# Optimization experiments

Measured on AMD Instinct MI355X. Metric: run time of the kernel, lower is better.

The kernel has to match this reference:

```python
import jax, jax.numpy as jnp
import numpy as np
import math

B, A, IN_C, OUT_C = 64, 128, 128, 64

def _l2norm(x, eps=1e-12):
    # matches F.normalize(dim=1) on 2D input: x / max(||x||_2, eps) along last dim
    n = jnp.sqrt(jnp.sum(x * x, axis=-1, keepdims=True))
    return x / jnp.maximum(n, eps)

def setup_inputs() -> dict:
    key = jax.random.key(0)
    ks = jax.random.split(key, 7)
    s = 1.0 / math.sqrt(IN_C)
    return {
        "features": jax.random.normal(ks[0], (B, IN_C, A), dtype=jnp.float32),
        "Wq": jax.random.uniform(ks[1], (OUT_C, IN_C), jnp.float32, -s, s),
        "bq": jax.random.uniform(ks[2], (OUT_C,), jnp.float32, -s, s),
        "Wk": jax.random.uniform(ks[3], (OUT_C, IN_C), jnp.float32, -s, s),
        "bk": jax.random.uniform(ks[4], (OUT_C,), jnp.float32, -s, s),
        "Wv": jax.random.uniform(ks[5], (OUT_C, IN_C), jnp.float32, -s, s),
        "bv": jax.random.uniform(ks[6], (OUT_C,), jnp.float32, -s, s),
    }

def reference(features, Wq, bq, Wk, bk, Wv, bv):
    b = features.shape[0]
    f = jnp.transpose(features, (0, 2, 1))          # (b, a, in_c)
    a = f.shape[1]
    q = f @ Wq.T + bq                               # (b, a, d)
    k = f @ Wk.T + bk
    v = f @ Wv.T + bv
    d = q.shape[-1]
    qf = q.reshape(-1, d)                           # (N, d), N = b*a
    kf = k.reshape(-1, d)
    vf = v.reshape(-1, d)
    att = jax.nn.softmax(qf @ kf.T / math.sqrt(d), axis=1)  # (N, N)
    qkv = att @ vf                                  # (N, d)
    qkv_n = _l2norm(qkv).reshape(b, a, d)
    v_n = _l2norm(vf).reshape(b, a, d)
    # sim_s[i,j] = (1/a) * sum_t v_n[i,t] . qkv_n[j,t]  (diagonal-trace over 'a')
    sim_s = jnp.einsum('bad,cad->bc', v_n, qkv_n) / a
    return sim_s
```

## Files before the change

### kernel.cpp

```cpp
#include <hip/hip_runtime.h>
#include <hip/hip_bf16.h>

#define NROW 8192
#define INC  128
#define OUTC 64
#define BG   16

#define QSCALE 0.18033688011112042f

typedef __bf16 bf16x8 __attribute__((ext_vector_type(8)));
typedef __bf16 bf16x4 __attribute__((ext_vector_type(4)));
typedef short  s16x4  __attribute__((ext_vector_type(4)));
typedef short  s16x8  __attribute__((ext_vector_type(8)));
typedef float  f32x4  __attribute__((ext_vector_type(4)));

static __device__ __forceinline__ f32x4 mfma16(bf16x8 a, bf16x8 b, f32x4 c) {
    return __builtin_amdgcn_mfma_f32_16x16x32_bf16(a, b, c, 0, 0, 0);
}
static __device__ __forceinline__ f32x4 mfma1k(s16x4 a, s16x4 b, f32x4 c) {
    return __builtin_amdgcn_mfma_f32_16x16x16bf16_1k(a, b, c, 0, 0, 0);
}

static __device__ __forceinline__ bf16x8 cvt8(float4 lo, float4 hi) {
    bf16x8 r;
    r[0] = (__bf16)lo.x; r[1] = (__bf16)lo.y; r[2] = (__bf16)lo.z; r[3] = (__bf16)lo.w;
    r[4] = (__bf16)hi.x; r[5] = (__bf16)hi.y; r[6] = (__bf16)hi.z; r[7] = (__bf16)hi.w;
    return r;
}
static __device__ __forceinline__ s16x4 vlo(s16x8 x) {
    return __builtin_shufflevector(x, x, 0, 1, 2, 3);
}
static __device__ __forceinline__ s16x4 vhi(s16x8 x) {
    return __builtin_shufflevector(x, x, 4, 5, 6, 7);
}

__global__ __launch_bounds__(256) void proj_kernel(
    const float* __restrict__ feat,
    const float* __restrict__ Wq, const float* __restrict__ bq,
    const float* __restrict__ Wk, const float* __restrict__ bk,
    const float* __restrict__ Wv, const float* __restrict__ bv,
    __hip_bfloat16* __restrict__ qbf, __hip_bfloat16* __restrict__ kbf,
    __hip_bfloat16* __restrict__ vbf, __hip_bfloat16* __restrict__ vnb)
{
    __shared__ float slab[32 * 132];
    __shared__ float vbuf[32 * 66];
    __shared__ float invb[32];

    const int blk = blockIdx.x;
    const int b   = blk >> 2;
    const int a0  = (blk & 3) * 32;
    const int r0  = b * 128 + a0;
    const float* fb = feat + (size_t)b * INC * 128;

    for (int i = threadIdx.x; i < 32 * 128; i += 256) {
        int c = i >> 5, a = i & 31;
        slab[a * 132 + c] = fb[c * 128 + a0 + a];
    }
    __syncthreads();

    const int w    = threadIdx.x >> 6;
    const int lane = threadIdx.x & 63;
    const int l16  = lane & 15;
    const int quad = lane >> 4;

    f32x4 acc[3][2];
    #pragma unroll
    for (int t = 0; t < 3; ++t)
        #pragma unroll
        for (int u = 0; u < 2; ++u)
            acc[t][u] = (f32x4){0.f, 0.f, 0.f, 0.f};

    #pragma unroll
    for (int kc = 0; kc < 4; ++kc) {
        const int k0 = kc * 32 + quad * 8;
        bf16x8 afr[2];
        #pragma unroll
        for (int u = 0; u < 2; ++u) {
            const float* ar = slab + (u * 16 + l16) * 132 + k0;
            afr[u] = cvt8(*(const float4*)ar, *(const float4*)(ar + 4));
        }
        #pragma unroll
        for (int t = 0; t < 3; ++t) {
            const int tile = w * 3 + t;
            const int mat  = tile >> 2;
            const float* W = (mat == 0) ? Wq : (mat == 1) ? Wk : Wv;
            const float* wr = W + ((tile & 3) * 16 + l16) * INC + k0;
            bf16x8 bfr = cvt8(*(const float4*)wr, *(const float4*)(wr + 4));
            #pragma unroll
            for (int u = 0; u < 2; ++u)
                acc[t][u] = mfma16(afr[u], bfr, acc[t][u]);
        }
    }

    #pragma unroll
    for (int t = 0; t < 3; ++t) {
        const int tile = w * 3 + t;
        const int mat  = tile >> 2;
        const int nt   = tile & 3;
        const float* bias = (mat == 0) ? bq : (mat == 1) ? bk : bv;
        const float bl = bias[nt * 16 + l16];
        if (mat == 0) {
            #pragma unroll
            for (int u = 0; u < 2; ++u) {
                const int base = ((((r0 >> 4) + u) * 4 + nt) << 8) + l16;
                #pragma unroll
                for (int r = 0; r < 4; ++r)
                    qbf[base + (quad * 4 + r) * 16] =
                        __float2bfloat16((acc[t][u][r] + bl) * QSCALE);
            }
        } else if (mat == 1) {
            const int kq = (r0 >> 5) * 2048 + (nt >> 1) * 512 +
                           ((nt & 1) * 2 + (l16 >> 3)) * 128 + quad * 32 + (l16 & 7);
            #pragma unroll
            for (int u = 0; u < 2; ++u)
                #pragma unroll
                for (int r = 0; r < 4; ++r)
                    kbf[kq + u * 1024 + r * 8] = __float2bfloat16(acc[t][u][r] + bl);
        } else {
            #pragma unroll
            for (int u = 0; u < 2; ++u)
                #pragma unroll
                for (int r = 0; r < 4; ++r)
                    vbuf[(u * 16 + quad * 4 + r) * 66 + nt * 16 + l16] = acc[t][u][r] + bl;
        }
    }
    __syncthreads();

    const int rl = threadIdx.x >> 3;
    const int jj = threadIdx.x & 7;
    float ss = 0.f;
    #pragma unroll
    for (int i = 0; i < 8; ++i) {
        float x = vbuf[rl * 66 + jj * 8 + i];
        ss += x * x;
    }
    ss += __shfl_xor(ss, 1, 64);
    ss += __shfl_xor(ss, 2, 64);
    ss += __shfl_xor(ss, 4, 64);
    if (jj == 0) invb[rl] = rsqrtf(fmaxf(ss, 1e-24f));
    __syncthreads();
    float inv = invb[rl];
    bf16x8 vp;
    #pragma unroll
    for (int i = 0; i < 8; ++i)
        vp[i] = (__bf16)(vbuf[rl * 66 + jj * 8 + i] * inv);
    *(bf16x8*)(vnb + (size_t)(r0 + rl) * 64 + jj * 8) = vp;

    const int tl = threadIdx.x & 15;
    const int n  = (threadIdx.x >> 4) & 3;
    const int s_ = threadIdx.x >> 6;
    bf16x8 pack;
    #pragma unroll
    for (int j = 0; j < 8; ++j) {
        int key = s_ * 8 + j;
        pack[j] = (__bf16)(vbuf[key * 66 + n * 16 + tl] * invb[key]);
    }
    const int e1 = (r0 >> 5) * 2048 + (s_ >> 1) * 1024 + (n >> 1) * 512 +
                   (s_ & 1) * 256 + tl * 8 + (n & 1) * 4;
    bf16x4 plo = __builtin_shufflevector(pack, pack, 0, 1, 2, 3);
    bf16x4 phi = __builtin_shufflevector(pack, pack, 4, 5, 6, 7);
    *(bf16x4*)(vbf + e1)       = plo;
    *(bf16x4*)(vbf + e1 + 128) = phi;
}

#define STAGE_W(BUF, KR, VR) do {                                            \
        *(float4*)((BUF) + stb) = KR;                                        \
        *(float4*)((BUF) + 4096 + stb) = VR; } while (0)
#define STAGE_L(KR, VR) do {                                                 \
        KR = *(const float4*)gk; VR = *(const float4*)gv;                    \
        gk += 4096; gv += 4096; } while (0)

#define COMPUTE(BUF) do {                                                    \
    const char* kbp = (BUF);                                                 \
    const char* vbp = (BUF) + 4096;                                          \
    bf16x8 k00 = *(const bf16x8*)(kbp + lb);                                 \
    bf16x8 k01 = *(const bf16x8*)(kbp + lb + 1024);                          \
    bf16x8 k10 = *(const bf16x8*)(kbp + lb + 2048);                          \
    bf16x8 k11 = *(const bf16x8*)(kbp + lb + 3072);                          \
    s16x8 W0 = *(const s16x8*)(vbp + lb);                                    \
    s16x8 W1 = *(const s16x8*)(vbp + lb + 1024);                             \
    s16x8 W2 = *(const s16x8*)(vbp + lb + 2048);                             \
    s16x8 W3 = *(const s16x8*)(vbp + lb + 3072);                             \
    const f32x4 zero = (f32x4){0.f, 0.f, 0.f, 0.f};                          \
    _Pragma("unroll")                                                        \
    for (int u = 0; u < 4; ++u) {                                            \
        f32x4 s0 = mfma16(k00, qf32[u][0], zero);                            \
        s0       = mfma16(k01, qf32[u][1], s0);                              \
        f32x4 s1 = mfma16(k10, qf32[u][0], zero);                            \
        s1       = mfma16(k11, qf32[u][1], s1);                              \
        union { bf16x4 v; s16x4 s; } pf0, pf1;                               \
        _Pragma("unroll")                                                    \
        for (int r = 0; r < 4; ++r) {                                        \
            float p0 = __builtin_amdgcn_exp2f(s0[r]);                        \
            float p1 = __builtin_amdgcn_exp2f(s1[r]);                        \
            lp[u] += p0 + p1;                                                \
            pf0.v[r] = (__bf16)p0;                                           \
            pf1.v[r] = (__bf16)p1;                                           \
        }                                                                    \
        of[u][0] = mfma1k(pf0.s, vlo(W0), of[u][0]);                         \
        of[u][0] = mfma1k(pf1.s, vlo(W2), of[u][0]);                         \
        of[u][1] = mfma1k(pf0.s, vhi(W0), of[u][1]);                         \
        of[u][1] = mfma1k(pf1.s, vhi(W2), of[u][1]);                         \
        of[u][2] = mfma1k(pf0.s, vlo(W1), of[u][2]);                         \
        of[u][2] = mfma1k(pf1.s, vlo(W3), of[u][2]);                         \
        of[u][3] = mfma1k(pf0.s, vhi(W1), of[u][3]);                         \
        of[u][3] = mfma1k(pf1.s, vhi(W3), of[u][3]);                         \
    } } while (0)

__global__ __launch_bounds__(256, 2) void attn_kernel(
    const __hip_bfloat16* __restrict__ qbf,
    const __hip_bfloat16* __restrict__ kbf,
    const __hip_bfloat16* __restrict__ vbf,
    float* __restrict__ Opart, float* __restrict__ lpart)
{
    __shared__ float4 ldsq[2][512];
    char* bufA = (char*)&ldsq[0][0];
    char* bufB = (char*)&ldsq[1][0];

    const int qb    = blockIdx.x >> 4;
    const int bg    = blockIdx.x & 15;
    const int tid   = threadIdx.x;
    const int w     = tid >> 6;
    const int lane  = tid & 63;
    const int l16   = lane & 15;
    const int quad  = lane >> 4;
    const int r0    = qb * 256 + w * 64;
    const int fo32  = l16 * 16 + (quad & 1) * 8;
    const int qh    = quad >> 1;
    const int lb    = lane * 16;
    const int stb   = tid * 16;

    bf16x8 qf32[4][2];
    #pragma unroll
    for (int u = 0; u < 4; ++u)
        #pragma unroll
        for (int p = 0; p < 2; ++p)
            qf32[u][p] = *(const bf16x8*)(qbf +
                ((((r0 >> 4) + u) * 4 + p * 2 + qh) << 8) + fo32);

    f32x4 of[4][4];
    float lp[4] = {0.f, 0.f, 0.f, 0.f};
    #pragma unroll
    for (int u = 0; u < 4; ++u)
        #pragma unroll
        for (int n = 0; n < 4; ++n)
            of[u][n] = (f32x4){0.f, 0.f, 0.f, 0.f};

    const char* gk = (const char*)kbf + (size_t)(bg * 16) * 4096 + stb;
    const char* gv = (const char*)vbf + (size_t)(bg * 16) * 4096 + stb;

    float4 ka, va, kb_, vb_;
    STAGE_L(ka, va);
    STAGE_W(bufA, ka, va);
    STAGE_L(kb_, vb_);
    __syncthreads();

    #pragma unroll 1
    for (int body = 0; body < 7; ++body) {
        STAGE_W(bufB, kb_, vb_);
        STAGE_L(ka, va);
        COMPUTE(bufA);
        __syncthreads();
        STAGE_W(bufA, ka, va);
        STAGE_L(kb_, vb_);
        COMPUTE(bufB);
        __syncthreads();
    }
    STAGE_W(bufB, kb_, vb_);
    COMPUTE(bufA);
    __syncthreads();
    COMPUTE(bufB);

    #pragma unroll
    for (int u = 0; u < 4; ++u) {
        float v = lp[u];
        v += __shfl_xor(v, 16, 64);
        v += __shfl_xor(v, 32, 64);
        lp[u] = v;
    }

    const int task = (qb * 4 + w) * 16 + bg;
    float* Ob = Opart + (size_t)task * 4096;
    #pragma unroll
    for (int u = 0; u < 4; ++u)
        #pragma unroll
        for (int n = 0; n < 4; ++n)
            #pragma unroll
            for (int r = 0; r < 4; ++r)
                Ob[(u * 16 + quad * 4 + r) * 64 + n * 16 + l16] = of[u][n][r];
    if (quad == 0) {
        #pragma unroll
        for (int u = 0; u < 4; ++u)
            lpart[task * 64 + u * 16 + l16] = lp[u];
    }
}

__global__ __launch_bounds__(256) void combine_kernel(
    const float* __restrict__ Opart, const float* __restrict__ lpart,
    __hip_bfloat16* __restrict__ qnb, float* __restrict__ outz)
{
    if (blockIdx.x == 0) {
        #pragma unroll
        for (int z = 0; z < 4; ++z)
            ((float4*)outz)[threadIdx.x * 4 + z] = (float4){0.f, 0.f, 0.f, 0.f};
    }

    const int r    = blockIdx.x * 4 + (threadIdx.x >> 6);
    const int c    = threadIdx.x & 63;
    const int tile = r >> 6, row = r & 63;
    float acc = 0.f, lsum = 0.f;
    #pragma unroll
    for (int g = 0; g < 16; ++g) {
        int task = tile * 16 + g;
        acc  += Opart[(size_t)task * 4096 + row * 64 + c];
        lsum += lpart[task * 64 + row];
    }
    float q = acc / lsum;
    float ss = q * q;
    ss += __shfl_xor(ss, 1, 64);
    ss += __shfl_xor(ss, 2, 64);
    ss += __shfl_xor(ss, 4, 64);
    ss += __shfl_xor(ss, 8, 64);
    ss += __shfl_xor(ss, 16, 64);
    ss += __shfl_xor(ss, 32, 64);
    qnb[(size_t)r * 64 + c] = __float2bfloat16(q * rsqrtf(fmaxf(ss, 1e-24f)));
}

__global__ __launch_bounds__(256) void sim_kernel(
    const __hip_bfloat16* __restrict__ vnb,
    const __hip_bfloat16* __restrict__ qnb,
    float* __restrict__ out)
{
    const int w    = threadIdx.x >> 6;
    const int lane = threadIdx.x & 63;
    const int l16  = lane & 15;
    const int quad = lane >> 4;
    const int k0   = blockIdx.x * 128 + w * 32 + quad * 8;

    f32x4 acc[4][4];
    #pragma unroll
    for (int mi = 0; mi < 4; ++mi)
        #pragma unroll
        for (int ni = 0; ni < 4; ++ni)
            acc[mi][ni] = (f32x4){0.f, 0.f, 0.f, 0.f};

    bf16x8 af[4], bfv[4];
    #pragma unroll
    for (int mi = 0; mi < 4; ++mi)
        af[mi] = *(const bf16x8*)(vnb + (size_t)(mi * 16 + l16) * 8192 + k0);
    #pragma unroll
    for (int ni = 0; ni < 4; ++ni)
        bfv[ni] = *(const bf16x8*)(qnb + (size_t)(ni * 16 + l16) * 8192 + k0);
    #pragma unroll
    for (int mi = 0; mi < 4; ++mi)
        #pragma unroll
        for (int ni = 0; ni < 4; ++ni)
            acc[mi][ni] = mfma16(af[mi], bfv[ni], acc[mi][ni]);

    #pragma unroll
    for (int mi = 0; mi < 4; ++mi)
        #pragma unroll
        for (int ni = 0; ni < 4; ++ni)
            #pragma unroll
            for (int r = 0; r < 4; ++r)
                atomicAdd(&out[(mi * 16 + quad * 4 + r) * 64 + ni * 16 + l16],
                          acc[mi][ni][r] * (1.f / 128.f));
}

extern "C" void kernel_launch(void* const* d_in, const int* in_sizes, int n_in,
                              void* d_out, int out_size, void* d_ws, size_t ws_size,
                              hipStream_t stream)
{
    const float* feat = (const float*)d_in[0];
    const float* Wq   = (const float*)d_in[1];
    const float* bq   = (const float*)d_in[2];
    const float* Wk   = (const float*)d_in[3];
    const float* bk   = (const float*)d_in[4];
    const float* Wv   = (const float*)d_in[5];
    const float* bv   = (const float*)d_in[6];
    float* out = (float*)d_out;

    const size_t MB = 1u << 20;
    char* ws = (char*)d_ws;
    __hip_bfloat16* qbf = (__hip_bfloat16*)(ws);
    __hip_bfloat16* kbf = (__hip_bfloat16*)(ws + 1 * MB);
    __hip_bfloat16* vbf = (__hip_bfloat16*)(ws + 2 * MB);
    __hip_bfloat16* vnb = (__hip_bfloat16*)(ws + 3 * MB);
    float* Opart = (float*)(ws + 4 * MB);
    float* lpart = (float*)(ws + 36 * MB);
    __hip_bfloat16* qnb = (__hip_bfloat16*)(ws + 37 * MB);

    proj_kernel<<<256, 256, 0, stream>>>(feat, Wq, bq, Wk, bk, Wv, bv, qbf, kbf, vbf, vnb);
    attn_kernel<<<512, 256, 0, stream>>>(qbf, kbf, vbf, Opart, lpart);
    combine_kernel<<<2048, 256, 0, stream>>>(Opart, lpart, qnb, out);
    sim_kernel<<<64, 256, 0, stream>>>(vnb, qnb, out);
}
```

Before: 121.6 us.

## Fuse all four stages into one cooperative kernel with grid syncs

Merges projection, attention, combine and similarity into a single cooperative launch of 512 blocks, separated by grid-wide barriers, and keeps the four-kernel path as a fallback if the cooperative launch fails. The aim is to remove the launch gaps and tail effects between the four kernel launches. The combine and similarity stages now run with fewer blocks looping over their work. Grid-sync cost and lower parallelism in the later stages may offset the savings.

```diff
diff --git a/kernel.cpp b/kernel.cpp
--- a/kernel.cpp
+++ b/kernel.cpp
@@ -1,5 +1,8 @@
 #include <hip/hip_runtime.h>
 #include <hip/hip_bf16.h>
+#include <hip/hip_cooperative_groups.h>
+
+namespace cg = cooperative_groups;
 
 #define NROW 8192
 #define INC  128
@@ -34,134 +37,6 @@
     return __builtin_shufflevector(x, x, 4, 5, 6, 7);
 }
 
-__global__ __launch_bounds__(256) void proj_kernel(
-    const float* __restrict__ feat,
-    const float* __restrict__ Wq, const float* __restrict__ bq,
-    const float* __restrict__ Wk, const float* __restrict__ bk,
-    const float* __restrict__ Wv, const float* __restrict__ bv,
-    __hip_bfloat16* __restrict__ qbf, __hip_bfloat16* __restrict__ kbf,
-    __hip_bfloat16* __restrict__ vbf, __hip_bfloat16* __restrict__ vnb)
-{
-    __shared__ float slab[32 * 132];
-    __shared__ float vbuf[32 * 66];
-    __shared__ float invb[32];
-
-    const int blk = blockIdx.x;
-    const int b   = blk >> 2;
-    const int a0  = (blk & 3) * 32;
-    const int r0  = b * 128 + a0;
-    const float* fb = feat + (size_t)b * INC * 128;
-
-    for (int i = threadIdx.x; i < 32 * 128; i += 256) {
-        int c = i >> 5, a = i & 31;
-        slab[a * 132 + c] = fb[c * 128 + a0 + a];
-    }
-    __syncthreads();
-
-    const int w    = threadIdx.x >> 6;
-    const int lane = threadIdx.x & 63;
-    const int l16  = lane & 15;
-    const int quad = lane >> 4;
-
-    f32x4 acc[3][2];
-    #pragma unroll
-    for (int t = 0; t < 3; ++t)
-        #pragma unroll
-        for (int u = 0; u < 2; ++u)
-            acc[t][u] = (f32x4){0.f, 0.f, 0.f, 0.f};
-
-    #pragma unroll
-    for (int kc = 0; kc < 4; ++kc) {
-        const int k0 = kc * 32 + quad * 8;
-        bf16x8 afr[2];
-        #pragma unroll
-        for (int u = 0; u < 2; ++u) {
-            const float* ar = slab + (u * 16 + l16) * 132 + k0;
-            afr[u] = cvt8(*(const float4*)ar, *(const float4*)(ar + 4));
-        }
-        #pragma unroll
-        for (int t = 0; t < 3; ++t) {
-            const int tile = w * 3 + t;
-            const int mat  = tile >> 2;
-            const float* W = (mat == 0) ? Wq : (mat == 1) ? Wk : Wv;
-            const float* wr = W + ((tile & 3) * 16 + l16) * INC + k0;
-            bf16x8 bfr = cvt8(*(const float4*)wr, *(const float4*)(wr + 4));
-            #pragma unroll
-            for (int u = 0; u < 2; ++u)
-                acc[t][u] = mfma16(afr[u], bfr, acc[t][u]);
-        }
-    }
-
-    #pragma unroll
-    for (int t = 0; t < 3; ++t) {
-        const int tile = w * 3 + t;
-        const int mat  = tile >> 2;
-        const int nt   = tile & 3;
-        const float* bias = (mat == 0) ? bq : (mat == 1) ? bk : bv;
-        const float bl = bias[nt * 16 + l16];
-        if (mat == 0) {
-            #pragma unroll
-            for (int u = 0; u < 2; ++u) {
-                const int base = ((((r0 >> 4) + u) * 4 + nt) << 8) + l16;
-                #pragma unroll
-                for (int r = 0; r < 4; ++r)
-                    qbf[base + (quad * 4 + r) * 16] =
-                        __float2bfloat16((acc[t][u][r] + bl) * QSCALE);
-            }
-        } else if (mat == 1) {
-            const int kq = (r0 >> 5) * 2048 + (nt >> 1) * 512 +
-                           ((nt & 1) * 2 + (l16 >> 3)) * 128 + quad * 32 + (l16 & 7);
-            #pragma unroll
-            for (int u = 0; u < 2; ++u)
-                #pragma unroll
-                for (int r = 0; r < 4; ++r)
-                    kbf[kq + u * 1024 + r * 8] = __float2bfloat16(acc[t][u][r] + bl);
-        } else {
-            #pragma unroll
-            for (int u = 0; u < 2; ++u)
-                #pragma unroll
-                for (int r = 0; r < 4; ++r)
-                    vbuf[(u * 16 + quad * 4 + r) * 66 + nt * 16 + l16] = acc[t][u][r] + bl;
-        }
-    }
-    __syncthreads();
-
-    const int rl = threadIdx.x >> 3;
-    const int jj = threadIdx.x & 7;
-    float ss = 0.f;
-    #pragma unroll
-    for (int i = 0; i < 8; ++i) {
-        float x = vbuf[rl * 66 + jj * 8 + i];
-        ss += x * x;
-    }
-    ss += __shfl_xor(ss, 1, 64);
-    ss += __shfl_xor(ss, 2, 64);
-    ss += __shfl_xor(ss, 4, 64);
-    if (jj == 0) invb[rl] = rsqrtf(fmaxf(ss, 1e-24f));
-    __syncthreads();
-    float inv = invb[rl];
-    bf16x8 vp;
-    #pragma unroll
-    for (int i = 0; i < 8; ++i)
-        vp[i] = (__bf16)(vbuf[rl * 66 + jj * 8 + i] * inv);
-    *(bf16x8*)(vnb + (size_t)(r0 + rl) * 64 + jj * 8) = vp;
-
-    const int tl = threadIdx.x & 15;
-    const int n  = (threadIdx.x >> 4) & 3;
-    const int s_ = threadIdx.x >> 6;
-    bf16x8 pack;
-    #pragma unroll
-    for (int j = 0; j < 8; ++j) {
-        int key = s_ * 8 + j;
-        pack[j] = (__bf16)(vbuf[key * 66 + n * 16 + tl] * invb[key]);
-    }
-    const int e1 = (r0 >> 5) * 2048 + (s_ >> 1) * 1024 + (n >> 1) * 512 +
-                   (s_ & 1) * 256 + tl * 8 + (n & 1) * 4;
-    bf16x4 plo = __builtin_shufflevector(pack, pack, 0, 1, 2, 3);
-    bf16x4 phi = __builtin_shufflevector(pack, pack, 4, 5, 6, 7);
-    *(bf16x4*)(vbf + e1)       = plo;
-    *(bf16x4*)(vbf + e1 + 128) = phi;
-}
 
 #define STAGE_W(BUF, KR, VR) do {                                            \
         *(float4*)((BUF) + stb) = KR;                                        \
@@ -207,92 +82,313 @@
         of[u][3] = mfma1k(pf1.s, vhi(W3), of[u][3]);                         \
     } } while (0)
 
+#define PROJ_BODY(BID)                                                       \
+    do {                                                                     \
+        const int b   = (BID) >> 2;                                          \
+        const int a0  = ((BID) & 3) * 32;                                    \
+        const int r0  = b * 128 + a0;                                        \
+        const float* fb = feat + (size_t)b * INC * 128;                      \
+        for (int i = tid; i < 32 * 128; i += 256) {                          \
+            int c = i >> 5, a = i & 31;                                      \
+            slab[a * 132 + c] = fb[c * 128 + a0 + a];                        \
+        }                                                                    \
+        __syncthreads();                                                     \
+        f32x4 acc[3][2];                                                     \
+        _Pragma("unroll")                                                    \
+        for (int t = 0; t < 3; ++t)                                          \
+            _Pragma("unroll")                                                \
+            for (int u = 0; u < 2; ++u)                                      \
+                acc[t][u] = (f32x4){0.f, 0.f, 0.f, 0.f};                     \
+        _Pragma("unroll")                                                    \
+        for (int kc = 0; kc < 4; ++kc) {                                     \
+            const int k0 = kc * 32 + quad * 8;                               \
+            bf16x8 afr[2];                                                   \
+            _Pragma("unroll")                                                \
+            for (int u = 0; u < 2; ++u) {                                    \
+                const float* ar = slab + (u * 16 + l16) * 132 + k0;          \
+                afr[u] = cvt8(*(const float4*)ar, *(const float4*)(ar + 4)); \
+            }                                                                \
+            _Pragma("unroll")                                                \
+            for (int t = 0; t < 3; ++t) {                                    \
+                const int tile = w * 3 + t;                                  \
+                const int mat  = tile >> 2;                                  \
+                const float* W = (mat == 0) ? Wq : (mat == 1) ? Wk : Wv;     \
+                const float* wr = W + ((tile & 3) * 16 + l16) * INC + k0;    \
+                bf16x8 bfr = cvt8(*(const float4*)wr, *(const float4*)(wr + 4)); \
+                _Pragma("unroll")                                            \
+                for (int u = 0; u < 2; ++u)                                  \
+                    acc[t][u] = mfma16(afr[u], bfr, acc[t][u]);              \
+            }                                                                \
+        }                                                                    \
+        _Pragma("unroll")                                                    \
+        for (int t = 0; t < 3; ++t) {                                        \
+            const int tile = w * 3 + t;                                      \
+            const int mat  = tile >> 2;                                      \
+            const int nt   = tile & 3;                                       \
+            const float* bias = (mat == 0) ? bq : (mat == 1) ? bk : bv;      \
+            const float bl = bias[nt * 16 + l16];                            \
+            if (mat == 0) {                                                  \
+                _Pragma("unroll")                                            \
+                for (int u = 0; u < 2; ++u) {                                \
+                    const int base = ((((r0 >> 4) + u) * 4 + nt) << 8) + l16;\
+                    _Pragma("unroll")                                        \
+                    for (int r = 0; r < 4; ++r)                              \
+                        qbf[base + (quad * 4 + r) * 16] =                    \
+                            __float2bfloat16((acc[t][u][r] + bl) * QSCALE);  \
+                }                                                            \
+            } else if (mat == 1) {                                           \
+                const int kq = (r0 >> 5) * 2048 + (nt >> 1) * 512 +          \
+                    ((nt & 1) * 2 + (l16 >> 3)) * 128 + quad * 32 + (l16 & 7);\
+                _Pragma("unroll")                                            \
+                for (int u = 0; u < 2; ++u)                                  \
+                    _Pragma("unroll")                                        \
+                    for (int r = 0; r < 4; ++r)                              \
+                        kbf[kq + u * 1024 + r * 8] =                         \
+                            __float2bfloat16(acc[t][u][r] + bl);             \
+            } else {                                                         \
+                _Pragma("unroll")                                            \
+                for (int u = 0; u < 2; ++u)                                  \
+                    _Pragma("unroll")                                        \
+                    for (int r = 0; r < 4; ++r)                              \
+                        vbuf[(u * 16 + quad * 4 + r) * 66 + nt * 16 + l16] = \
+                            acc[t][u][r] + bl;                               \
+            }                                                                \
+        }                                                                    \
+        __syncthreads();                                                     \
+        const int rl = tid >> 3;                                             \
+        const int jj = tid & 7;                                              \
+        float ss = 0.f;                                                      \
+        _Pragma("unroll")                                                    \
+        for (int i = 0; i < 8; ++i) {                                        \
+            float x = vbuf[rl * 66 + jj * 8 + i];                            \
+            ss += x * x;                                                     \
+        }                                                                    \
+        ss += __shfl_xor(ss, 1, 64);                                         \
+        ss += __shfl_xor(ss, 2, 64);                                         \
+        ss += __shfl_xor(ss, 4, 64);                                         \
+        if (jj == 0) invb[rl] = rsqrtf(fmaxf(ss, 1e-24f));                   \
+        __syncthreads();                                                     \
+        float inv = invb[rl];                                                \
+        bf16x8 vpk;                                                          \
+        _Pragma("unroll")                                                    \
+        for (int i = 0; i < 8; ++i)                                          \
+            vpk[i] = (__bf16)(vbuf[rl * 66 + jj * 8 + i] * inv);             \
+        *(bf16x8*)(vnb + (size_t)(r0 + rl) * 64 + jj * 8) = vpk;             \
+        const int tl = tid & 15;                                             \
+        const int n  = (tid >> 4) & 3;                                       \
+        const int s_ = tid >> 6;                                             \
+        bf16x8 pack;                                                         \
+        _Pragma("unroll")                                                    \
+        for (int j = 0; j < 8; ++j) {                                        \
+            int key = s_ * 8 + j;                                            \
+            pack[j] = (__bf16)(vbuf[key * 66 + n * 16 + tl] * invb[key]);    \
+        }                                                                    \
+        const int e1 = (r0 >> 5) * 2048 + (s_ >> 1) * 1024 + (n >> 1) * 512 +\
+                       (s_ & 1) * 256 + tl * 8 + (n & 1) * 4;                \
+        bf16x4 plo = __builtin_shufflevector(pack, pack, 0, 1, 2, 3);        \
+        bf16x4 phi = __builtin_shufflevector(pack, pack, 4, 5, 6, 7);        \
+        *(bf16x4*)(vbf + e1)       = plo;                                    \
+        *(bf16x4*)(vbf + e1 + 128) = phi;                                    \
+    } while (0)
+
+#define ATTN_BODY(BID, BUFA, BUFB)                                           \
+    do {                                                                     \
+        const int qb   = (BID) >> 4;                                         \
+        const int bg   = (BID) & 15;                                         \
+        const int r0   = qb * 256 + w * 64;                                  \
+        const int fo32 = l16 * 16 + (quad & 1) * 8;                          \
+        const int qh   = quad >> 1;                                          \
+        const int lb   = lane * 16;                                          \
+        const int stb  = tid * 16;                                           \
+        bf16x8 qf32[4][2];                                                   \
+        _Pragma("unroll")                                                    \
+        for (int u = 0; u < 4; ++u)                                          \
+            _Pragma("unroll")                                                \
+            for (int p = 0; p < 2; ++p)                                      \
+                qf32[u][p] = *(const bf16x8*)(qbf +                          \
+                    ((((r0 >> 4) + u) * 4 + p * 2 + qh) << 8) + fo32);       \
+        f32x4 of[4][4];                                                      \
+        float lp[4] = {0.f, 0.f, 0.f, 0.f};                                  \
+        _Pragma("unroll")                                                    \
+        for (int u = 0; u < 4; ++u)                                          \
+            _Pragma("unroll")                                                \
+            for (int n = 0; n < 4; ++n)                                      \
+                of[u][n] = (f32x4){0.f, 0.f, 0.f, 0.f};                      \
+        const char* gk = (const char*)kbf + (size_t)(bg * 16) * 4096 + stb;  \
+        const char* gv = (const char*)vbf + (size_t)(bg * 16) * 4096 + stb;  \
+        float4 ka, va, kb_, vb_;                                             \
+        STAGE_L(ka, va);                                                     \
+        STAGE_W(BUFA, ka, va);                                               \
+        STAGE_L(kb_, vb_);                                                   \
+        __syncthreads();                                                     \
+        _Pragma("unroll 1")                                                  \
+        for (int body = 0; body < 7; ++body) {                               \
+            STAGE_W(BUFB, kb_, vb_);                                         \
+            STAGE_L(ka, va);                                                 \
+            COMPUTE(BUFA);                                                   \
+            __syncthreads();                                                 \
+            STAGE_W(BUFA, ka, va);                                           \
+            STAGE_L(kb_, vb_);                                               \
+            COMPUTE(BUFB);                                                   \
+            __syncthreads();                                                 \
+        }                                                                    \
+        STAGE_W(BUFB, kb_, vb_);                                             \
+        COMPUTE(BUFA);                                                       \
+        __syncthreads();                                                     \
+        COMPUTE(BUFB);                                                       \
+        _Pragma("unroll")                                                    \
+        for (int u = 0; u < 4; ++u) {                                        \
+            float v = lp[u];                                                 \
+            v += __shfl_xor(v, 16, 64);                                      \
+            v += __shfl_xor(v, 32, 64);                                      \
+            lp[u] = v;                                                       \
+        }                                                                    \
+        const int task = (qb * 4 + w) * 16 + bg;                             \
+        float* Ob = Opart + (size_t)task * 4096;                             \
+        _Pragma("unroll")                                                    \
+        for (int u = 0; u < 4; ++u)                                          \
+            _Pragma("unroll")                                                \
+            for (int n = 0; n < 4; ++n)                                      \
+                _Pragma("unroll")                                            \
+                for (int r = 0; r < 4; ++r)                                  \
+                    Ob[(u * 16 + quad * 4 + r) * 64 + n * 16 + l16] =        \
+                        of[u][n][r];                                         \
+        if (quad == 0) {                                                     \
+            _Pragma("unroll")                                                \
+            for (int u = 0; u < 4; ++u)                                      \
+                lpart[task * 64 + u * 16 + l16] = lp[u];                     \
+        }                                                                    \
+    } while (0)
+
+__global__ __launch_bounds__(256, 2) void mega_kernel(
+    const float* __restrict__ feat,
+    const float* __restrict__ Wq, const float* __restrict__ bq,
+    const float* __restrict__ Wk, const float* __restrict__ bk,
+    const float* __restrict__ Wv, const float* __restrict__ bv,
+    __hip_bfloat16* __restrict__ qbf, __hip_bfloat16* __restrict__ kbf,
+    __hip_bfloat16* __restrict__ vbf, __hip_bfloat16* __restrict__ vnb,
+    float* __restrict__ Opart, float* __restrict__ lpart,
+    __hip_bfloat16* __restrict__ qnb, float* __restrict__ out)
+{
+    cg::grid_group gg = cg::this_grid();
+
+    __shared__ __align__(16) char pool[25472];
+
+    const int bid = blockIdx.x;
+    const int tid = threadIdx.x;
+    const int w    = tid >> 6;
+    const int lane = tid & 63;
+    const int l16  = lane & 15;
+    const int quad = lane >> 4;
+
+    if (bid < 256) {
+        float* slab = (float*)pool;
+        float* vbuf = (float*)(pool + 16896);
+        float* invb = (float*)(pool + 25344);
+        PROJ_BODY(bid);
+    }
+    __threadfence();
+    gg.sync();
+
+    {
+        char* bufA = pool;
+        char* bufB = pool + 8192;
+        ATTN_BODY(bid, bufA, bufB);
+    }
+    __threadfence();
+    gg.sync();
+
+    {
+        if (bid == 0) {
+            #pragma unroll
+            for (int z = 0; z < 4; ++z)
+                ((float4*)out)[tid * 4 + z] = (float4){0.f, 0.f, 0.f, 0.f};
+        }
+        #pragma unroll 1
+        for (int it = 0; it < 4; ++it) {
+            const int r    = (it * 512 + bid) * 4 + (tid >> 6);
+            const int c    = tid & 63;
+            const int tile = r >> 6, row = r & 63;
+            float acc = 0.f, lsum = 0.f;
+            #pragma unroll
+            for (int g = 0; g < 16; ++g) {
+                int task = tile * 16 + g;
+                acc  += Opart[(size_t)task * 4096 + row * 64 + c];
+                lsum += lpart[task * 64 + row];
+            }
+            float q = acc / lsum;
+            float ss = q * q;
+            ss += __shfl_xor(ss, 1, 64);
+            ss += __shfl_xor(ss, 2, 64);
+            ss += __shfl_xor(ss, 4, 64);
+            ss += __shfl_xor(ss, 8, 64);
+            ss += __shfl_xor(ss, 16, 64);
+            ss += __shfl_xor(ss, 32, 64);
+            qnb[(size_t)r * 64 + c] = __float2bfloat16(q * rsqrtf(fmaxf(ss, 1e-24f)));
+        }
+    }
+    __threadfence();
+    gg.sync();
+
+    if (bid < 256) {
+        const int k0 = bid * 32 + quad * 8;
+        f32x4 acc[4];
+        #pragma unroll
+        for (int ni = 0; ni < 4; ++ni)
+            acc[ni] = (f32x4){0.f, 0.f, 0.f, 0.f};
+
+        bf16x8 af = *(const bf16x8*)(vnb + (size_t)(w * 16 + l16) * 8192 + k0);
+        bf16x8 bfv[4];
+        #pragma unroll
+        for (int ni = 0; ni < 4; ++ni)
+            bfv[ni] = *(const bf16x8*)(qnb + (size_t)(ni * 16 + l16) * 8192 + k0);
+        #pragma unroll
+        for (int ni = 0; ni < 4; ++ni)
+            acc[ni] = mfma16(af, bfv[ni], acc[ni]);
+
+        #pragma unroll
+        for (int ni = 0; ni < 4; ++ni)
+            #pragma unroll
+            for (int r = 0; r < 4; ++r)
+                atomicAdd(&out[(w * 16 + quad * 4 + r) * 64 + ni * 16 + l16],
+                          acc[ni][r] * (1.f / 128.f));
+    }
+}
+
+__global__ __launch_bounds__(256) void proj_kernel(
+    const float* __restrict__ feat,
+    const float* __restrict__ Wq, const float* __restrict__ bq,
+    const float* __restrict__ Wk, const float* __restrict__ bk,
+    const float* __restrict__ Wv, const float* __restrict__ bv,
+    __hip_bfloat16* __restrict__ qbf, __hip_bfloat16* __restrict__ kbf,
+    __hip_bfloat16* __restrict__ vbf, __hip_bfloat16* __restrict__ vnb)
+{
+    __shared__ float slab[32 * 132];
+    __shared__ float vbuf[32 * 66];
+    __shared__ float invb[32];
+    const int tid = threadIdx.x;
+    const int w    = tid >> 6;
+    const int lane = tid & 63;
+    const int l16  = lane & 15;
+    const int quad = lane >> 4;
+    PROJ_BODY(blockIdx.x);
+}
+
 __global__ __launch_bounds__(256, 2) void attn_kernel(
     const __hip_bfloat16* __restrict__ qbf,
     const __hip_bfloat16* __restrict__ kbf,
     const __hip_bfloat16* __restrict__ vbf,
     float* __restrict__ Opart, float* __restrict__ lpart)
 {
-    __shared__ float4 ldsq[2][512];
-    char* bufA = (char*)&ldsq[0][0];
-    char* bufB = (char*)&ldsq[1][0];
-
-    const int qb    = blockIdx.x >> 4;
-    const int bg    = blockIdx.x & 15;
-    const int tid   = threadIdx.x;
-    const int w     = tid >> 6;
-    const int lane  = tid & 63;
-    const int l16   = lane & 15;
-    const int quad  = lane >> 4;
-    const int r0    = qb * 256 + w * 64;
-    const int fo32  = l16 * 16 + (quad & 1) * 8;
-    const int qh    = quad >> 1;
-    const int lb    = lane * 16;
-    const int stb   = tid * 16;
-
-    bf16x8 qf32[4][2];
-    #pragma unroll
-    for (int u = 0; u < 4; ++u)
-        #pragma unroll
-        for (int p = 0; p < 2; ++p)
-            qf32[u][p] = *(const bf16x8*)(qbf +
-                ((((r0 >> 4) + u) * 4 + p * 2 + qh) << 8) + fo32);
-
-    f32x4 of[4][4];
-    float lp[4] = {0.f, 0.f, 0.f, 0.f};
-    #pragma unroll
-    for (int u = 0; u < 4; ++u)
-        #pragma unroll
-        for (int n = 0; n < 4; ++n)
-            of[u][n] = (f32x4){0.f, 0.f, 0.f, 0.f};
-
-    const char* gk = (const char*)kbf + (size_t)(bg * 16) * 4096 + stb;
-    const char* gv = (const char*)vbf + (size_t)(bg * 16) * 4096 + stb;
-
-    float4 ka, va, kb_, vb_;
-    STAGE_L(ka, va);
-    STAGE_W(bufA, ka, va);
-    STAGE_L(kb_, vb_);
-    __syncthreads();
-
-    #pragma unroll 1
-    for (int body = 0; body < 7; ++body) {
-        STAGE_W(bufB, kb_, vb_);
-        STAGE_L(ka, va);
-        COMPUTE(bufA);
-        __syncthreads();
-        STAGE_W(bufA, ka, va);
-        STAGE_L(kb_, vb_);
-        COMPUTE(bufB);
-        __syncthreads();
-    }
-    STAGE_W(bufB, kb_, vb_);
-    COMPUTE(bufA);
-    __syncthreads();
-    COMPUTE(bufB);
-
-    #pragma unroll
-    for (int u = 0; u < 4; ++u) {
-        float v = lp[u];
-        v += __shfl_xor(v, 16, 64);
-        v += __shfl_xor(v, 32, 64);
-        lp[u] = v;
-    }
-
-    const int task = (qb * 4 + w) * 16 + bg;
-    float* Ob = Opart + (size_t)task * 4096;
-    #pragma unroll
-    for (int u = 0; u < 4; ++u)
-        #pragma unroll
-        for (int n = 0; n < 4; ++n)
-            #pragma unroll
-            for (int r = 0; r < 4; ++r)
-                Ob[(u * 16 + quad * 4 + r) * 64 + n * 16 + l16] = of[u][n][r];
-    if (quad == 0) {
-        #pragma unroll
-        for (int u = 0; u < 4; ++u)
-            lpart[task * 64 + u * 16 + l16] = lp[u];
-    }
+    __shared__ __align__(16) char pool[16384];
+    const int tid = threadIdx.x;
+    const int w    = tid >> 6;
+    const int lane = tid & 63;
+    const int l16  = lane & 15;
+    const int quad = lane >> 4;
+    char* bufA = pool;
+    char* bufB = pool + 8192;
+    ATTN_BODY(blockIdx.x, bufA, bufB);
 }
 
 __global__ __launch_bounds__(256) void combine_kernel(
@@ -304,7 +400,6 @@
         for (int z = 0; z < 4; ++z)
             ((float4*)outz)[threadIdx.x * 4 + z] = (float4){0.f, 0.f, 0.f, 0.f};
     }
-
     const int r    = blockIdx.x * 4 + (threadIdx.x >> 6);
     const int c    = threadIdx.x & 63;
     const int tile = r >> 6, row = r & 63;
@@ -390,8 +485,18 @@
     float* lpart = (float*)(ws + 36 * MB);
     __hip_bfloat16* qnb = (__hip_bfloat16*)(ws + 37 * MB);
 
-    proj_kernel<<<256, 256, 0, stream>>>(feat, Wq, bq, Wk, bk, Wv, bv, qbf, kbf, vbf, vnb);
-    attn_kernel<<<512, 256, 0, stream>>>(qbf, kbf, vbf, Opart, lpart);
-    combine_kernel<<<2048, 256, 0, stream>>>(Opart, lpart, qnb, out);
-    sim_kernel<<<64, 256, 0, stream>>>(vnb, qnb, out);
-}
+    void* args[] = {
+        (void*)&feat, (void*)&Wq, (void*)&bq, (void*)&Wk, (void*)&bk,
+        (void*)&Wv, (void*)&bv, (void*)&qbf, (void*)&kbf, (void*)&vbf,
+        (void*)&vnb, (void*)&Opart, (void*)&lpart, (void*)&qnb, (void*)&out
+    };
+    hipError_t err = hipLaunchCooperativeKernel((const void*)mega_kernel,
+                                                dim3(512), dim3(256), args, 0, stream);
+    if (err != hipSuccess) {
+        proj_kernel<<<256, 256, 0, stream>>>(feat, Wq, bq, Wk, bk, Wv, bv,
+                                             qbf, kbf, vbf, vnb);
+        attn_kernel<<<512, 256, 0, stream>>>(qbf, kbf, vbf, Opart, lpart);
+        combine_kernel<<<2048, 256, 0, stream>>>(Opart, lpart, qnb, out);
+        sim_kernel<<<64, 256, 0, stream>>>(vnb, qnb, out);
+    }
+}
```

Result: slower. 443.2 us (+264.4%).

## Fuse split-K combine with similarity kernel and relayout partial outputs

Applied to the files above, without the earlier changes.

Merges the combine and similarity kernels into one finish kernel that, per position a, reduces the 16 split partials for all 64 batches, normalizes them into shared memory, and immediately runs the MFMA similarity contraction. Opart/lpart are stored row-major with the split index inner, so each reduction reads contiguous float4s, and the output zeroing moves into the attention kernel. This removes one launch and the qnb round trip through global memory. The cost is more atomics to the output (128 blocks each adding 64x64 values) and fewer blocks in the final stage.

```diff
diff --git a/kernel.cpp b/kernel.cpp
--- a/kernel.cpp
+++ b/kernel.cpp
@@ -46,22 +46,22 @@
     __shared__ float vbuf[32 * 66];
     __shared__ float invb[32];
 
-    const int blk = blockIdx.x;
-    const int b   = blk >> 2;
-    const int a0  = (blk & 3) * 32;
+    const int tid = threadIdx.x;
+    const int w    = tid >> 6;
+    const int lane = tid & 63;
+    const int l16  = lane & 15;
+    const int quad = lane >> 4;
+
+    const int b   = blockIdx.x >> 2;
+    const int a0  = (blockIdx.x & 3) * 32;
     const int r0  = b * 128 + a0;
     const float* fb = feat + (size_t)b * INC * 128;
 
-    for (int i = threadIdx.x; i < 32 * 128; i += 256) {
+    for (int i = tid; i < 32 * 128; i += 256) {
         int c = i >> 5, a = i & 31;
         slab[a * 132 + c] = fb[c * 128 + a0 + a];
     }
     __syncthreads();
-
-    const int w    = threadIdx.x >> 6;
-    const int lane = threadIdx.x & 63;
-    const int l16  = lane & 15;
-    const int quad = lane >> 4;
 
     f32x4 acc[3][2];
     #pragma unroll
@@ -126,8 +126,8 @@
     }
     __syncthreads();
 
-    const int rl = threadIdx.x >> 3;
-    const int jj = threadIdx.x & 7;
+    const int rl = tid >> 3;
+    const int jj = tid & 7;
     float ss = 0.f;
     #pragma unroll
     for (int i = 0; i < 8; ++i) {
@@ -140,15 +140,15 @@
     if (jj == 0) invb[rl] = rsqrtf(fmaxf(ss, 1e-24f));
     __syncthreads();
     float inv = invb[rl];
-    bf16x8 vp;
+    bf16x8 vpk;
     #pragma unroll
     for (int i = 0; i < 8; ++i)
-        vp[i] = (__bf16)(vbuf[rl * 66 + jj * 8 + i] * inv);
-    *(bf16x8*)(vnb + (size_t)(r0 + rl) * 64 + jj * 8) = vp;
-
-    const int tl = threadIdx.x & 15;
-    const int n  = (threadIdx.x >> 4) & 3;
-    const int s_ = threadIdx.x >> 6;
+        vpk[i] = (__bf16)(vbuf[rl * 66 + jj * 8 + i] * inv);
+    *(bf16x8*)(vnb + (size_t)(r0 + rl) * 64 + jj * 8) = vpk;
+
+    const int tl = tid & 15;
+    const int n  = (tid >> 4) & 3;
+    const int s_ = tid >> 6;
     bf16x8 pack;
     #pragma unroll
     for (int j = 0; j < 8; ++j) {
@@ -211,24 +211,31 @@
     const __hip_bfloat16* __restrict__ qbf,
     const __hip_bfloat16* __restrict__ kbf,
     const __hip_bfloat16* __restrict__ vbf,
-    float* __restrict__ Opart, float* __restrict__ lpart)
+    float* __restrict__ Opart, float* __restrict__ lpart,
+    float* __restrict__ outz)
 {
-    __shared__ float4 ldsq[2][512];
-    char* bufA = (char*)&ldsq[0][0];
-    char* bufB = (char*)&ldsq[1][0];
-
-    const int qb    = blockIdx.x >> 4;
-    const int bg    = blockIdx.x & 15;
-    const int tid   = threadIdx.x;
-    const int w     = tid >> 6;
-    const int lane  = tid & 63;
-    const int l16   = lane & 15;
-    const int quad  = lane >> 4;
-    const int r0    = qb * 256 + w * 64;
-    const int fo32  = l16 * 16 + (quad & 1) * 8;
-    const int qh    = quad >> 1;
-    const int lb    = lane * 16;
-    const int stb   = tid * 16;
+    __shared__ __align__(16) char pool[16384];
+    char* bufA = pool;
+    char* bufB = pool + 8192;
+
+    const int tid = threadIdx.x;
+    if (blockIdx.x == 0) {
+        #pragma unroll
+        for (int z = 0; z < 4; ++z)
+            ((float4*)outz)[tid * 4 + z] = (float4){0.f, 0.f, 0.f, 0.f};
+    }
+
+    const int w    = tid >> 6;
+    const int lane = tid & 63;
+    const int l16  = lane & 15;
+    const int quad = lane >> 4;
+    const int qb   = blockIdx.x >> 4;
+    const int bg   = blockIdx.x & 15;
+    const int r0   = qb * 256 + w * 64;
+    const int fo32 = l16 * 16 + (quad & 1) * 8;
+    const int qh   = quad >> 1;
+    const int lb   = lane * 16;
+    const int stb  = tid * 16;
 
     bf16x8 qf32[4][2];
     #pragma unroll
@@ -279,92 +286,91 @@
         lp[u] = v;
     }
 
-    const int task = (qb * 4 + w) * 16 + bg;
-    float* Ob = Opart + (size_t)task * 4096;
     #pragma unroll
     for (int u = 0; u < 4; ++u)
         #pragma unroll
         for (int n = 0; n < 4; ++n)
             #pragma unroll
             for (int r = 0; r < 4; ++r)
-                Ob[(u * 16 + quad * 4 + r) * 64 + n * 16 + l16] = of[u][n][r];
+                Opart[((size_t)(r0 + u * 16 + quad * 4 + r) * 16 + bg) * 64
+                      + n * 16 + l16] = of[u][n][r];
     if (quad == 0) {
         #pragma unroll
         for (int u = 0; u < 4; ++u)
-            lpart[task * 64 + u * 16 + l16] = lp[u];
-    }
-}
-
-__global__ __launch_bounds__(256) void combine_kernel(
+            lpart[(r0 + u * 16 + l16) * 16 + bg] = lp[u];
+    }
+}
+
+__global__ __launch_bounds__(512) void finish_kernel(
     const float* __restrict__ Opart, const float* __restrict__ lpart,
-    __hip_bfloat16* __restrict__ qnb, float* __restrict__ outz)
-{
-    if (blockIdx.x == 0) {
-        #pragma unroll
-        for (int z = 0; z < 4; ++z)
-            ((float4*)outz)[threadIdx.x * 4 + z] = (float4){0.f, 0.f, 0.f, 0.f};
-    }
-
-    const int r    = blockIdx.x * 4 + (threadIdx.x >> 6);
-    const int c    = threadIdx.x & 63;
-    const int tile = r >> 6, row = r & 63;
-    float acc = 0.f, lsum = 0.f;
-    #pragma unroll
-    for (int g = 0; g < 16; ++g) {
-        int task = tile * 16 + g;
-        acc  += Opart[(size_t)task * 4096 + row * 64 + c];
-        lsum += lpart[task * 64 + row];
-    }
-    float q = acc / lsum;
-    float ss = q * q;
-    ss += __shfl_xor(ss, 1, 64);
-    ss += __shfl_xor(ss, 2, 64);
-    ss += __shfl_xor(ss, 4, 64);
-    ss += __shfl_xor(ss, 8, 64);
-    ss += __shfl_xor(ss, 16, 64);
-    ss += __shfl_xor(ss, 32, 64);
-    qnb[(size_t)r * 64 + c] = __float2bfloat16(q * rsqrtf(fmaxf(ss, 1e-24f)));
-}
-
-__global__ __launch_bounds__(256) void sim_kernel(
     const __hip_bfloat16* __restrict__ vnb,
-    const __hip_bfloat16* __restrict__ qnb,
     float* __restrict__ out)
 {
-    const int w    = threadIdx.x >> 6;
-    const int lane = threadIdx.x & 63;
-    const int l16  = lane & 15;
-    const int quad = lane >> 4;
-    const int k0   = blockIdx.x * 128 + w * 32 + quad * 8;
-
-    f32x4 acc[4][4];
-    #pragma unroll
-    for (int mi = 0; mi < 4; ++mi)
-        #pragma unroll
-        for (int ni = 0; ni < 4; ++ni)
-            acc[mi][ni] = (f32x4){0.f, 0.f, 0.f, 0.f};
-
-    bf16x8 af[4], bfv[4];
-    #pragma unroll
-    for (int mi = 0; mi < 4; ++mi)
-        af[mi] = *(const bf16x8*)(vnb + (size_t)(mi * 16 + l16) * 8192 + k0);
-    #pragma unroll
-    for (int ni = 0; ni < 4; ++ni)
-        bfv[ni] = *(const bf16x8*)(qnb + (size_t)(ni * 16 + l16) * 8192 + k0);
-    #pragma unroll
-    for (int mi = 0; mi < 4; ++mi)
-        #pragma unroll
-        for (int ni = 0; ni < 4; ++ni)
-            acc[mi][ni] = mfma16(af[mi], bfv[ni], acc[mi][ni]);
-
-    #pragma unroll
-    for (int mi = 0; mi < 4; ++mi)
+    __shared__ __hip_bfloat16 qn[64][68];
+
+    const int a   = blockIdx.x;
+    const int tid = threadIdx.x;
+
+    {
+        const int b  = tid >> 3;
+        const int c8 = tid & 7;
+        const int r  = b * 128 + a;
+        float acc[8] = {0.f, 0.f, 0.f, 0.f, 0.f, 0.f, 0.f, 0.f};
+        #pragma unroll
+        for (int g = 0; g < 16; ++g) {
+            const float* src = Opart + ((size_t)r * 16 + g) * 64 + c8 * 8;
+            float4 t0 = *(const float4*)(src);
+            float4 t1 = *(const float4*)(src + 4);
+            acc[0] += t0.x; acc[1] += t0.y; acc[2] += t0.z; acc[3] += t0.w;
+            acc[4] += t1.x; acc[5] += t1.y; acc[6] += t1.z; acc[7] += t1.w;
+        }
+        float lsum = lpart[r * 16 + c8 * 2] + lpart[r * 16 + c8 * 2 + 1];
+        lsum += __shfl_xor(lsum, 1, 64);
+        lsum += __shfl_xor(lsum, 2, 64);
+        lsum += __shfl_xor(lsum, 4, 64);
+        const float inv_l = 1.0f / lsum;
+        float ss = 0.f;
+        #pragma unroll
+        for (int c = 0; c < 8; ++c) {
+            acc[c] *= inv_l;
+            ss += acc[c] * acc[c];
+        }
+        ss += __shfl_xor(ss, 1, 64);
+        ss += __shfl_xor(ss, 2, 64);
+        ss += __shfl_xor(ss, 4, 64);
+        const float inv = rsqrtf(fmaxf(ss, 1e-24f));
+        bf16x8 pk;
+        #pragma unroll
+        for (int c = 0; c < 8; ++c)
+            pk[c] = (__bf16)(acc[c] * inv);
+        *(bf16x8*)&qn[b][c8 * 8] = pk;
+    }
+    __syncthreads();
+
+    {
+        const int w    = tid >> 6;
+        const int lane = tid & 63;
+        const int l16  = lane & 15;
+        const int quad = lane >> 4;
+        const int ks   = w & 1;
+        const int mi   = w >> 1;
+        const int dq   = ks * 32 + quad * 8;
+
+        bf16x8 af = *(const bf16x8*)(vnb +
+            (size_t)(mi * 16 + l16) * 8192 + a * 64 + dq);
+        f32x4 accd[4];
+        #pragma unroll
+        for (int ni = 0; ni < 4; ++ni) {
+            bf16x8 bfv = *(const bf16x8*)&qn[ni * 16 + l16][dq];
+            accd[ni] = mfma16(af, bfv, (f32x4){0.f, 0.f, 0.f, 0.f});
+        }
         #pragma unroll
         for (int ni = 0; ni < 4; ++ni)
             #pragma unroll
             for (int r = 0; r < 4; ++r)
                 atomicAdd(&out[(mi * 16 + quad * 4 + r) * 64 + ni * 16 + l16],
-                          acc[mi][ni][r] * (1.f / 128.f));
+                          accd[ni][r] * (1.f / 128.f));
+    }
 }
 
 extern "C" void kernel_launch(void* const* d_in, const int* in_sizes, int n_in,
@@ -388,10 +394,9 @@
     __hip_bfloat16* vnb = (__hip_bfloat16*)(ws + 3 * MB);
     float* Opart = (float*)(ws + 4 * MB);
     float* lpart = (float*)(ws + 36 * MB);
-    __hip_bfloat16* qnb = (__hip_bfloat16*)(ws + 37 * MB);
-
-    proj_kernel<<<256, 256, 0, stream>>>(feat, Wq, bq, Wk, bk, Wv, bv, qbf, kbf, vbf, vnb);
-    attn_kernel<<<512, 256, 0, stream>>>(qbf, kbf, vbf, Opart, lpart);
-    combine_kernel<<<2048, 256, 0, stream>>>(Opart, lpart, qnb, out);
-    sim_kernel<<<64, 256, 0, stream>>>(vnb, qnb, out);
-}
+
+    proj_kernel<<<256, 256, 0, stream>>>(feat, Wq, bq, Wk, bk, Wv, bv,
+                                         qbf, kbf, vbf, vnb);
+    attn_kernel<<<512, 256, 0, stream>>>(qbf, kbf, vbf, Opart, lpart, out);
+    finish_kernel<<<128, 512, 0, stream>>>(Opart, lpart, vnb, out);
+}
```

Measured after the change: 113.9 us. -6.4%, faster.
